# Kernel tuning notes

Measured on AMD Instinct MI355X. Metric: run time of the kernel, lower is better.

## Reference

```python
import jax, jax.numpy as jnp
import numpy as np

B, C, S, E, H = 16, 24, 128, 256, 8
P = E // H  # head projection dim (consistent interpretation of the buggy source)
EPS = 1e-6


def _ln(x, g, b):
    mu = jnp.mean(x, axis=-1, keepdims=True)
    var = jnp.mean((x - mu) ** 2, axis=-1, keepdims=True)
    return (x - mu) * jax.lax.rsqrt(var + EPS) * g + b


def setup_inputs() -> dict:
    key = jax.random.key(0)
    ks = jax.random.split(key, 16)
    s = 0.02
    return {
        'x': jax.random.normal(ks[0], (B, C, S, E), jnp.float32),
        # spatial attention params
        'Wq_s': s * jax.random.normal(ks[1], (H, C, P, E), jnp.float32),
        'Wk_s': s * jax.random.normal(ks[2], (H, E, P), jnp.float32),
        'Wv_s': s * jax.random.normal(ks[3], (H, E, P), jnp.float32),
        'Wo_s': s * jax.random.normal(ks[4], (C, E, E), jnp.float32),
        # temporal attention params
        'Wq_t': s * jax.random.normal(ks[5], (H, C, E, P), jnp.float32),
        'Wk_t': s * jax.random.normal(ks[6], (H, C, E, P), jnp.float32),
        'Wv_t': s * jax.random.normal(ks[7], (H, C, E, P), jnp.float32),
        'Wo_t': s * jax.random.normal(ks[8], (C, E, E), jnp.float32),
        # shared layernorm
        'ln_g': jnp.ones((E,), jnp.float32),
        'ln_b': jnp.zeros((E,), jnp.float32),
        # per-joint pointwise FF (Linear->ReLU->Linear)
        'ff_w1': s * jax.random.normal(ks[9], (C, E, E), jnp.float32),
        'ff_b1': jnp.zeros((C, E), jnp.float32),
        'ff_w2': s * jax.random.normal(ks[10], (C, E, E), jnp.float32),
        'ff_b2': jnp.zeros((C, E), jnp.float32),
    }


def _spatial_attention(x, Wq, Wk, Wv, Wo):
    # x: [B,C,S,E]; per-head per-joint query proj, shared key/value proj
    q = jnp.einsum('bcse,hcpe->bshcp', x, Wq)          # [B,S,H,C,P]
    k = jnp.einsum('bcse,hep->bshcp', x, Wk)
    v = jnp.einsum('bcse,hep->bshcp', x, Wv)
    scores = jnp.einsum('bshcp,bshdp->bshcd', q, k) / jnp.sqrt(jnp.float32(P))
    a = jax.nn.softmax(scores, axis=-1)                # attn over joints d
    o = jnp.einsum('bshcd,bshdp->bshcp', a, v)
    o = o.transpose(0, 3, 1, 2, 4).reshape(x.shape[0], C, x.shape[2], H * P)  # [B,C,S,E]
    return jnp.einsum('bcse,cef->bcsf', o, Wo)


def _temporal_attention(x, Wq, Wk, Wv, Wo):
    q = jnp.einsum('bcse,hcep->bhcsp', x, Wq)          # [B,H,C,S,P]
    k = jnp.einsum('bcse,hcep->bhcsp', x, Wk)
    v = jnp.einsum('bcse,hcep->bhcsp', x, Wv)
    scores = jnp.einsum('bhcsp,bhctp->bhcst', q, k) / jnp.sqrt(jnp.float32(P))
    a = jax.nn.softmax(scores, axis=-1)                # attn over time t
    o = jnp.einsum('bhcst,bhctp->bhcsp', a, v)
    o = o.transpose(0, 2, 3, 1, 4).reshape(x.shape[0], C, x.shape[2], H * P)  # [B,C,S,E]
    return jnp.einsum('bcse,cef->bcsf', o, Wo)


def reference(x, Wq_s, Wk_s, Wv_s, Wo_s, Wq_t, Wk_t, Wv_t, Wo_t, ln_g, ln_b, ff_w1, ff_b1, ff_w2, ff_b2):
    spat = _spatial_attention(x, Wq_s, Wk_s, Wv_s, Wo_s)
    temp = _temporal_attention(x, Wq_t, Wk_t, Wv_t, Wo_t)
    attn_out = _ln(x + spat, ln_g, ln_b) + _ln(x + temp, ln_g, ln_b)
    # per-joint pointwise FF, vectorized over joints
    h = jax.nn.relu(jnp.einsum('bcse,cef->bcsf', attn_out, ff_w1) + ff_b1[None, :, None, :])
    ff = jnp.einsum('bcse,cef->bcsf', h, ff_w2) + ff_b2[None, :, None, :]
    return _ln(attn_out + ff, ln_g, ln_b)
```

## Files before the change

### kernel.cpp

```cpp
#include <hip/hip_runtime.h>
#include <hip/hip_bf16.h>

constexpr int Bn = 16, Cn = 24, Sn = 128, En = 256, Hn = 8, Pn = 32;
constexpr int NROWS = Bn * Cn * Sn;
constexpr size_t NBUF = (size_t)Bn * Cn * Sn * En;
constexpr size_t WSLOT = (size_t)Cn * 256 * 256;

typedef __bf16 bf16_t;
typedef bf16_t bf16x8 __attribute__((ext_vector_type(8)));
typedef bf16_t bf16x4 __attribute__((ext_vector_type(4)));
typedef float f32x4 __attribute__((ext_vector_type(4)));

__device__ __forceinline__ void gl2lds16(const bf16_t* g, bf16_t* l) {
    typedef const __attribute__((address_space(1))) unsigned int* gp_t;
    typedef __attribute__((address_space(3))) unsigned int* lp_t;
    __builtin_amdgcn_global_load_lds((gp_t)(unsigned long long)g,
                                     (lp_t)(unsigned int)(unsigned long long)l,
                                     16, 0, 0);
}

__global__ __launch_bounds__(256) void conv_x_k(const float* __restrict__ x,
                                                bf16_t* __restrict__ xb) {
    const size_t i = ((size_t)blockIdx.x * 256 + threadIdx.x) * 4;
    const float4 v = *(const float4*)(x + i);
    bf16x4 o = {(bf16_t)v.x, (bf16_t)v.y, (bf16_t)v.z, (bf16_t)v.w};
    *(bf16x4*)(xb + i) = o;
}

__global__ __launch_bounds__(256) void conv_w_copy_k(const float* __restrict__ W,
                                                     bf16_t* __restrict__ out) {
    const int row = blockIdx.x * 4 + (threadIdx.x >> 6);
    const int lane = threadIdx.x & 63;
    const int n = row & 255, c = row >> 8;
    const float* src = W + (size_t)c * (Pn * En) + (size_t)(n >> 5) * (Cn * Pn * En) +
                       (size_t)(n & 31) * En + lane * 4;
    const float4 v = *(const float4*)src;
    bf16x4 o = {(bf16_t)v.x, (bf16_t)v.y, (bf16_t)v.z, (bf16_t)v.w};
    *(bf16x4*)(out + (size_t)row * 256 + lane * 4) = o;
}

struct TDesc { const float* W; int Sc, Snh, Se; };

__global__ __launch_bounds__(256) void conv_w_tr_k(
    TDesc d0, TDesc d1, TDesc d2, TDesc d3, TDesc d4, TDesc d5, TDesc d6,
    bf16_t* __restrict__ out)
{
    TDesc d;
    switch (blockIdx.z) {
        case 0: d = d0; break; case 1: d = d1; break; case 2: d = d2; break;
        case 3: d = d3; break; case 4: d = d4; break; case 5: d = d5; break;
        default: d = d6; break;
    }
    const int g = blockIdx.x & 7, et = blockIdx.x >> 3;
    const int c = blockIdx.y;

    __shared__ float tile[32][65];

    const int t = threadIdx.x;
    const float* base = d.W + (size_t)c * d.Sc + (size_t)g * d.Snh;

#pragma unroll
    for (int pass = 0; pass < 2; ++pass) {
        const int e_local = pass * 32 + (t >> 3);
        const int j4 = (t & 7) * 4;
        const float4 v = *(const float4*)(base + (size_t)(et * 64 + e_local) * d.Se + j4);
        tile[j4 + 0][e_local] = v.x;
        tile[j4 + 1][e_local] = v.y;
        tile[j4 + 2][e_local] = v.z;
        tile[j4 + 3][e_local] = v.w;
    }
    __syncthreads();

    const int j = t >> 3, e8 = (t & 7) * 8;
    bf16x8 o;
#pragma unroll
    for (int k = 0; k < 8; ++k) o[k] = (bf16_t)tile[j][e8 + k];
    *(bf16x8*)(out + (size_t)blockIdx.z * WSLOT +
               ((size_t)c * 256 + g * 32 + j) * 256 + et * 64 + e8) = o;
}

__global__ __launch_bounds__(256) void conv_w_k(const float* __restrict__ W,
                                                bf16_t* __restrict__ Wb,
                                                int Sc, int Snh, int Snp, int Se) {
    const int n = blockIdx.x & 255, c = blockIdx.x >> 8;
    const int e = threadIdx.x;
    Wb[(size_t)blockIdx.x * 256 + e] =
        (bf16_t)W[(size_t)c * Sc + (size_t)(n >> 5) * Snh + (n & 31) * Snp + (size_t)e * Se];
}

struct GDesc { const bf16_t* W; bf16_t* O; int Wc, Ob, Oc, Os, Onh, Onp, trans; };

template <int NP, int EPI>
__global__ __launch_bounds__(256) void gemm_mfma(
    const bf16_t* __restrict__ A, int Ab, int Ac, int As,
    GDesc g0, GDesc g1, GDesc g2, const float* __restrict__ bias)
{
    const int b = blockIdx.x, c = blockIdx.z;
    const int proj = (NP == 1) ? 0 : ((int)blockIdx.y >> 1);
    const int nt = (NP == 1) ? (int)blockIdx.y : ((int)blockIdx.y & 1);
    GDesc g = (proj == 0) ? g0 : (proj == 1) ? g1 : g2;

    __shared__ bf16_t smem[2][2][128 * 32];
    bf16_t* Cs = &smem[0][0][0];

    const int tid = threadIdx.x, wv = tid >> 6, ln = tid & 63;
    const int wm = (wv >> 1) * 64, wn = (wv & 1) * 64;
    const int lr = ln & 15, hi = ln >> 4, lk = hi * 8;

    const bf16_t* Abase = A + (size_t)b * Ab + (size_t)c * Ac;
    const bf16_t* Bbase = g.W + (size_t)c * g.Wc + (size_t)(nt * 128) * 256;

    auto stage = [&](int buf, int k0) {
#pragma unroll
        for (int it = 0; it < 2; ++it) {
            const int cb = it * 256 + wv * 64;
            const int mc = cb + ln;
            const int row = mc >> 2, kc = (mc & 3) * 8;
            gl2lds16(Abase + (size_t)row * As + k0 + kc, &smem[buf][0][cb * 8]);
            gl2lds16(Bbase + (size_t)row * 256 + k0 + kc, &smem[buf][1][cb * 8]);
        }
    };

    f32x4 acc[4][4] = {};

    stage(0, 0);
    __syncthreads();

#pragma unroll
    for (int kt = 0; kt < 8; ++kt) {
        const int cur = kt & 1;
        if (kt < 7) stage(cur ^ 1, (kt + 1) * 32);

        bf16x8 af[4], bfr[4];
#pragma unroll
        for (int i = 0; i < 4; ++i)
            af[i] = *(const bf16x8*)&smem[cur][0][(wm + i * 16 + lr) * 32 + lk];
#pragma unroll
        for (int j = 0; j < 4; ++j)
            bfr[j] = *(const bf16x8*)&smem[cur][1][(wn + j * 16 + lr) * 32 + lk];
#pragma unroll
        for (int i = 0; i < 4; ++i)
#pragma unroll
            for (int j = 0; j < 4; ++j)
                acc[i][j] = __builtin_amdgcn_mfma_f32_16x16x32_bf16(af[i], bfr[j], acc[i][j], 0, 0, 0);

        __syncthreads();
    }

#pragma unroll
    for (int pass = 0; pass < 2; ++pass) {
        if (!g.trans) {
            if (wm == pass * 64) {
#pragma unroll
                for (int i = 0; i < 4; ++i)
#pragma unroll
                    for (int j = 0; j < 4; ++j) {
                        const int n = nt * 128 + wn + j * 16 + lr;
                        float bv = 0.f;
                        if (EPI) bv = bias[c * 256 + n];
#pragma unroll
                        for (int r = 0; r < 4; ++r) {
                            float v = acc[i][j][r];
                            if (EPI) { v += bv; if (EPI == 1) v = fmaxf(v, 0.f); }
                            Cs[(i * 16 + hi * 4 + r) * 136 + wn + j * 16 + lr] = (bf16_t)v;
                        }
                    }
            }
            __syncthreads();
#pragma unroll
            for (int it = 0; it < 2; ++it) {
                const int lrow = it * 32 + (tid >> 3);
                const int n0 = (tid & 7) * 16;
                bf16x8 v0 = *(const bf16x8*)&Cs[lrow * 136 + n0];
                bf16x8 v1 = *(const bf16x8*)&Cs[lrow * 136 + n0 + 8];
                const int m = pass * 64 + lrow;
                const int n = nt * 128 + n0;
                bf16_t* dst = g.O + (size_t)b * g.Ob + (size_t)c * g.Oc +
                              (size_t)m * g.Os + (size_t)(n >> 5) * g.Onh + (n & 31);
                *(bf16x8*)dst = v0;
                *(bf16x8*)(dst + 8) = v1;
            }
            __syncthreads();
        } else {
            if (wn == pass * 64) {
#pragma unroll
                for (int i = 0; i < 4; ++i)
#pragma unroll
                    for (int j = 0; j < 4; ++j) {
                        bf16x4 pk = {(bf16_t)acc[i][j][0], (bf16_t)acc[i][j][1],
                                     (bf16_t)acc[i][j][2], (bf16_t)acc[i][j][3]};
                        *(bf16x4*)&Cs[(j * 16 + lr) * 136 + wm + i * 16 + hi * 4] = pk;
                    }
            }
            __syncthreads();
#pragma unroll
            for (int it = 0; it < 2; ++it) {
                const int lrow = it * 32 + (tid >> 3);
                const int m0 = (tid & 7) * 16;
                bf16x8 v0 = *(const bf16x8*)&Cs[lrow * 136 + m0];
                bf16x8 v1 = *(const bf16x8*)&Cs[lrow * 136 + m0 + 8];
                const int n = nt * 128 + pass * 64 + lrow;
                bf16_t* dst = g.O + (size_t)b * g.Ob + (size_t)c * g.Oc +
                              (size_t)(n >> 5) * g.Onh + (size_t)(n & 31) * g.Onp + m0;
                *(bf16x8*)dst = v0;
                *(bf16x8*)(dst + 8) = v1;
            }
            __syncthreads();
        }
    }
}

__global__ __launch_bounds__(256) void attn_spatial_mfma(
    const bf16_t* __restrict__ Q, const bf16_t* __restrict__ K,
    const bf16_t* __restrict__ V, bf16_t* __restrict__ O)
{
    __shared__ bf16_t Ps[4][32 * 40];
    __shared__ bf16_t Vt[4][32 * 40];

    const int tid = threadIdx.x, wv = tid >> 6, ln = tid & 63;
    const int lr = ln & 15, hi = ln >> 4, lk = hi * 8;

    const int bsh = blockIdx.x * 4 + wv;
    const int h = bsh & 7, s = (bsh >> 3) & 127, b = bsh >> 10;
    const size_t qb = (size_t)bsh * (Cn * Pn);

    {
        const int p = ln >> 1, c0 = 24 + (ln & 1) * 4;
        bf16x4 z = {};
        *(bf16x4*)&Vt[wv][p * 40 + c0] = z;
    }
#pragma unroll
    for (int it = 0; it < 2; ++it) {
        const int ch = it * 64 + ln;
        if (ch < 96) {
            const int cc = ch >> 2, p0 = (ch & 3) * 8;
            bf16x8 v = *(const bf16x8*)(V + qb + cc * 32 + p0);
#pragma unroll
            for (int j = 0; j < 8; ++j)
                Vt[wv][(p0 + j) * 40 + cc] = v[j];
        }
    }

    bf16x8 aq0 = *(const bf16x8*)(Q + qb + lr * 32 + lk);
    bf16x8 aq1 = *(const bf16x8*)(Q + qb + (16 + lr) * 32 + lk);
    bf16x8 bk0 = *(const bf16x8*)(K + qb + lr * 32 + lk);
    bf16x8 bk1 = *(const bf16x8*)(K + qb + (16 + lr) * 32 + lk);
    const f32x4 zz = {0.f, 0.f, 0.f, 0.f};
    f32x4 sc[2][2];
    sc[0][0] = __builtin_amdgcn_mfma_f32_16x16x32_bf16(aq0, bk0, zz, 0, 0, 0);
    sc[0][1] = __builtin_amdgcn_mfma_f32_16x16x32_bf16(aq0, bk1, zz, 0, 0, 0);
    sc[1][0] = __builtin_amdgcn_mfma_f32_16x16x32_bf16(aq1, bk0, zz, 0, 0, 0);
    sc[1][1] = __builtin_amdgcn_mfma_f32_16x16x32_bf16(aq1, bk1, zz, 0, 0, 0);

    const float scale = 0.17677669529663687f;
#pragma unroll
    for (int i = 0; i < 2; ++i) {
        float s0[4], s1[4], mx[4];
#pragma unroll
        for (int r = 0; r < 4; ++r) {
            s0[r] = sc[i][0][r] * scale;
            s1[r] = (lr >= 8) ? -3.0e38f : sc[i][1][r] * scale;
            mx[r] = fmaxf(s0[r], s1[r]);
        }
#pragma unroll
        for (int d = 1; d < 16; d <<= 1)
#pragma unroll
            for (int r = 0; r < 4; ++r) mx[r] = fmaxf(mx[r], __shfl_xor(mx[r], d));
        float e0[4], e1[4], sm[4];
#pragma unroll
        for (int r = 0; r < 4; ++r) {
            e0[r] = __expf(s0[r] - mx[r]);
            e1[r] = __expf(s1[r] - mx[r]);
            sm[r] = e0[r] + e1[r];
        }
#pragma unroll
        for (int d = 1; d < 16; d <<= 1)
#pragma unroll
            for (int r = 0; r < 4; ++r) sm[r] += __shfl_xor(sm[r], d);
#pragma unroll
        for (int r = 0; r < 4; ++r) {
            const float inv = 1.f / sm[r];
            const int row = i * 16 + hi * 4 + r;
            Ps[wv][row * 40 + lr]      = (bf16_t)(e0[r] * inv);
            Ps[wv][row * 40 + 16 + lr] = (bf16_t)(e1[r] * inv);
        }
    }

    bf16x8 ap0 = *(const bf16x8*)&Ps[wv][lr * 40 + lk];
    bf16x8 ap1 = *(const bf16x8*)&Ps[wv][(16 + lr) * 40 + lk];
    bf16x8 bv0 = *(const bf16x8*)&Vt[wv][lr * 40 + lk];
    bf16x8 bv1 = *(const bf16x8*)&Vt[wv][(16 + lr) * 40 + lk];
    f32x4 o[2][2];
    o[0][0] = __builtin_amdgcn_mfma_f32_16x16x32_bf16(ap0, bv0, zz, 0, 0, 0);
    o[0][1] = __builtin_amdgcn_mfma_f32_16x16x32_bf16(ap0, bv1, zz, 0, 0, 0);
    o[1][0] = __builtin_amdgcn_mfma_f32_16x16x32_bf16(ap1, bv0, zz, 0, 0, 0);
    o[1][1] = __builtin_amdgcn_mfma_f32_16x16x32_bf16(ap1, bv1, zz, 0, 0, 0);

#pragma unroll
    for (int i = 0; i < 2; ++i)
#pragma unroll
        for (int r = 0; r < 4; ++r) {
            const int c = i * 16 + hi * 4 + r;
            if (c < 24) {
                const size_t ob = ((size_t)(b * Cn + c) * Sn + s) * En + h * Pn;
#pragma unroll
                for (int j = 0; j < 2; ++j)
                    O[ob + j * 16 + lr] = (bf16_t)o[i][j][r];
            }
        }
}

__global__ __launch_bounds__(256) void attn_temporal_mfma(
    const bf16_t* __restrict__ Q, const bf16_t* __restrict__ K,
    const bf16_t* __restrict__ Vt, bf16_t* __restrict__ O)
{
    const int c = blockIdx.x, h = blockIdx.y, b = blockIdx.z;
    const size_t base = ((size_t)(b * Hn + h) * Cn + c) * (Sn * Pn);

    __shared__ bf16_t Qs[128 * 32];
    __shared__ bf16_t Ks[128 * 32];
    __shared__ bf16_t Vs[32 * 136];
    __shared__ bf16_t Ps[128 * 136];

    const int tid = threadIdx.x, wv = tid >> 6, ln = tid & 63;
    const int lr = ln & 15, lk = (ln >> 4) * 8;

#pragma unroll
    for (int it = 0; it < 2; ++it) {
        const int cb = it * 256 + wv * 64;
        const int mc = cb + ln;
        const int row = mc >> 2, kc = (mc & 3) * 8;
        gl2lds16(Q + base + row * 32 + kc, &Qs[cb * 8]);
        gl2lds16(K + base + row * 32 + kc, &Ks[cb * 8]);
    }
#pragma unroll
    for (int it = 0; it < 2; ++it) {
        const int mc = it * 256 + tid;
        const int p = mc >> 4, scn = (mc & 15) * 8;
        bf16x8 v = *(const bf16x8*)(Vt + base + p * 128 + scn);
        *(bf16x8*)&Vs[p * 136 + scn] = v;
    }
    __syncthreads();

    const int r0 = wv * 32;
    bf16x8 aq0 = *(const bf16x8*)&Qs[(r0 + lr) * 32 + lk];
    bf16x8 aq1 = *(const bf16x8*)&Qs[(r0 + 16 + lr) * 32 + lk];
    f32x4 sc_[2][8];
    const f32x4 zz = {0.f, 0.f, 0.f, 0.f};
#pragma unroll
    for (int j = 0; j < 8; ++j) {
        bf16x8 bk = *(const bf16x8*)&Ks[(j * 16 + lr) * 32 + lk];
        sc_[0][j] = __builtin_amdgcn_mfma_f32_16x16x32_bf16(aq0, bk, zz, 0, 0, 0);
        sc_[1][j] = __builtin_amdgcn_mfma_f32_16x16x32_bf16(aq1, bk, zz, 0, 0, 0);
    }

    const float scale = 0.17677669529663687f;
#pragma unroll
    for (int i = 0; i < 2; ++i) {
        float mx[4], sm[4];
#pragma unroll
        for (int r = 0; r < 4; ++r) {
            float m = sc_[i][0][r];
#pragma unroll
            for (int j = 1; j < 8; ++j) m = fmaxf(m, sc_[i][j][r]);
            mx[r] = m;
        }
#pragma unroll
        for (int d = 1; d < 16; d <<= 1)
#pragma unroll
            for (int r = 0; r < 4; ++r) mx[r] = fmaxf(mx[r], __shfl_xor(mx[r], d));
#pragma unroll
        for (int r = 0; r < 4; ++r) sm[r] = 0.f;
#pragma unroll
        for (int j = 0; j < 8; ++j)
#pragma unroll
            for (int r = 0; r < 4; ++r) {
                const float e = __expf((sc_[i][j][r] - mx[r]) * scale);
                sc_[i][j][r] = e; sm[r] += e;
            }
#pragma unroll
        for (int d = 1; d < 16; d <<= 1)
#pragma unroll
            for (int r = 0; r < 4; ++r) sm[r] += __shfl_xor(sm[r], d);
        float inv[4];
#pragma unroll
        for (int r = 0; r < 4; ++r) inv[r] = 1.f / sm[r];
        const int rb = r0 + i * 16 + (ln >> 4) * 4;
#pragma unroll
        for (int j = 0; j < 8; ++j)
#pragma unroll
            for (int r = 0; r < 4; ++r)
                Ps[(rb + r) * 136 + j * 16 + lr] = (bf16_t)(sc_[i][j][r] * inv[r]);
    }
    __syncthreads();

    f32x4 o[2][2] = {};
#pragma unroll
    for (int kk = 0; kk < 4; ++kk) {
        bf16x8 ap0 = *(const bf16x8*)&Ps[(r0 + lr) * 136 + kk * 32 + lk];
        bf16x8 ap1 = *(const bf16x8*)&Ps[(r0 + 16 + lr) * 136 + kk * 32 + lk];
        bf16x8 bv0 = *(const bf16x8*)&Vs[lr * 136 + kk * 32 + lk];
        bf16x8 bv1 = *(const bf16x8*)&Vs[(16 + lr) * 136 + kk * 32 + lk];
        o[0][0] = __builtin_amdgcn_mfma_f32_16x16x32_bf16(ap0, bv0, o[0][0], 0, 0, 0);
        o[0][1] = __builtin_amdgcn_mfma_f32_16x16x32_bf16(ap0, bv1, o[0][1], 0, 0, 0);
        o[1][0] = __builtin_amdgcn_mfma_f32_16x16x32_bf16(ap1, bv0, o[1][0], 0, 0, 0);
        o[1][1] = __builtin_amdgcn_mfma_f32_16x16x32_bf16(ap1, bv1, o[1][1], 0, 0, 0);
    }

#pragma unroll
    for (int i = 0; i < 2; ++i) {
        const int sb = r0 + i * 16 + (ln >> 4) * 4;
#pragma unroll
        for (int j = 0; j < 2; ++j) {
            const int p = h * 32 + j * 16 + lr;
#pragma unroll
            for (int r = 0; r < 4; ++r)
                O[((size_t)(b * Cn + c) * Sn + (sb + r)) * En + p] = (bf16_t)o[i][j][r];
        }
    }
}

__global__ __launch_bounds__(256) void ln_combine_k(
    const bf16_t* __restrict__ xb, const bf16_t* __restrict__ spat,
    const bf16_t* __restrict__ temp, const float* __restrict__ g,
    const float* __restrict__ beta, bf16_t* __restrict__ AO)
{
    const int row = blockIdx.x * 4 + (threadIdx.x >> 6);
    const int lane = threadIdx.x & 63;
    const size_t off = (size_t)row * En;

    float v1[4], v2[4];
    float s1 = 0, s2 = 0, q1 = 0, q2 = 0;
#pragma unroll
    for (int i = 0; i < 4; i++) {
        const int e = lane + i * 64;
        const float xv = (float)xb[off + e];
        const float a = xv + (float)spat[off + e];
        const float t = xv + (float)temp[off + e];
        v1[i] = a; v2[i] = t;
        s1 += a; s2 += t; q1 += a * a; q2 += t * t;
    }
    for (int d = 32; d; d >>= 1) {
        s1 += __shfl_xor(s1, d); s2 += __shfl_xor(s2, d);
        q1 += __shfl_xor(q1, d); q2 += __shfl_xor(q2, d);
    }
    const float mu1 = s1 / En, mu2 = s2 / En;
    const float r1 = rsqrtf(q1 / En - mu1 * mu1 + 1e-6f);
    const float r2 = rsqrtf(q2 / En - mu2 * mu2 + 1e-6f);
#pragma unroll
    for (int i = 0; i < 4; i++) {
        const int e = lane + i * 64;
        const float out = (v1[i] - mu1) * r1 * g[e] + beta[e] +
                          (v2[i] - mu2) * r2 * g[e] + beta[e];
        AO[off + e] = (bf16_t)out;
    }
}

__global__ __launch_bounds__(256) void ln_final_k(
    const bf16_t* __restrict__ AO, const bf16_t* __restrict__ FF,
    const float* __restrict__ g, const float* __restrict__ beta,
    float* __restrict__ out)
{
    const int row = blockIdx.x * 4 + (threadIdx.x >> 6);
    const int lane = threadIdx.x & 63;
    const size_t off = (size_t)row * En;

    float v[4];
    float s = 0, q = 0;
#pragma unroll
    for (int i = 0; i < 4; i++) {
        const int e = lane + i * 64;
        const float a = (float)AO[off + e] + (float)FF[off + e];
        v[i] = a; s += a; q += a * a;
    }
    for (int d = 32; d; d >>= 1) { s += __shfl_xor(s, d); q += __shfl_xor(q, d); }
    const float mu = s / En;
    const float r = rsqrtf(q / En - mu * mu + 1e-6f);
#pragma unroll
    for (int i = 0; i < 4; i++) {
        const int e = lane + i * 64;
        out[off + e] = (v[i] - mu) * r * g[e] + beta[e];
    }
}

extern "C" void kernel_launch(void* const* d_in, const int* in_sizes, int n_in,
                              void* d_out, int out_size, void* d_ws, size_t ws_size,
                              hipStream_t stream)
{
    const float* x     = (const float*)d_in[0];
    const float* Wq_s  = (const float*)d_in[1];
    const float* Wk_s  = (const float*)d_in[2];
    const float* Wv_s  = (const float*)d_in[3];
    const float* Wo_s  = (const float*)d_in[4];
    const float* Wq_t  = (const float*)d_in[5];
    const float* Wk_t  = (const float*)d_in[6];
    const float* Wv_t  = (const float*)d_in[7];
    const float* Wo_t  = (const float*)d_in[8];
    const float* ln_g  = (const float*)d_in[9];
    const float* ln_b  = (const float*)d_in[10];
    const float* ff_w1 = (const float*)d_in[11];
    const float* ff_b1 = (const float*)d_in[12];
    const float* ff_w2 = (const float*)d_in[13];
    const float* ff_b2 = (const float*)d_in[14];
    float* out = (float*)d_out;

    bf16_t* wsb = (bf16_t*)d_ws;
    bf16_t* b0 = wsb;
    bf16_t* b1 = wsb + NBUF;
    bf16_t* b2 = wsb + 2 * NBUF;
    bf16_t* b3 = wsb + 3 * NBUF;
    bf16_t* b4 = wsb + 4 * NBUF;

    bf16_t* xb = (bf16_t*)d_out;
    bf16_t* wb = xb + NBUF;
    bf16_t* w_qs = wb + 0 * WSLOT;
    bf16_t* wtr  = wb + 1 * WSLOT;
    bf16_t* w_os = wtr + 0 * WSLOT;
    bf16_t* w_qt = wtr + 1 * WSLOT;
    bf16_t* w_kt = wtr + 2 * WSLOT;
    bf16_t* w_vt = wtr + 3 * WSLOT;
    bf16_t* w_ot = wtr + 4 * WSLOT;
    bf16_t* w_f1 = wtr + 5 * WSLOT;
    bf16_t* w_f2 = wtr + 6 * WSLOT;
    bf16_t* w_ks = b4 + NBUF - 2 * 65536;
    bf16_t* w_vs = b4 + NBUF - 65536;

    const int XAb = Cn * Sn * En, XAc = Sn * En, XAs = En;
    const int QSb = Sn * Hn * Cn * Pn, QSs = Hn * Cn * Pn, QSh = Cn * Pn;
    const int QTb = Hn * Cn * Sn * Pn, QTh = Cn * Sn * Pn, QTc = Sn * Pn, QTs = Pn;
    const int WCP = 256 * 256;

    conv_x_k<<<NBUF / 1024, 256, 0, stream>>>(x, xb);
    conv_w_copy_k<<<1536, 256, 0, stream>>>(Wq_s, w_qs);
    conv_w_tr_k<<<dim3(32, 24, 7), 256, 0, stream>>>(
        TDesc{Wo_s, En * En, Pn, En},
        TDesc{Wq_t, En * Pn, Cn * En * Pn, Pn},
        TDesc{Wk_t, En * Pn, Cn * En * Pn, Pn},
        TDesc{Wv_t, En * Pn, Cn * En * Pn, Pn},
        TDesc{Wo_t, En * En, Pn, En},
        TDesc{ff_w1, En * En, Pn, En},
        TDesc{ff_w2, En * En, Pn, En},
        wtr);
    conv_w_k<<<256, 256, 0, stream>>>(Wk_s, w_ks, 0, En * Pn, 1, Pn);
    conv_w_k<<<256, 256, 0, stream>>>(Wv_s, w_vs, 0, En * Pn, 1, Pn);

    gemm_mfma<3, 0><<<dim3(16, 6, 24), 256, 0, stream>>>(
        xb, XAb, XAc, XAs,
        GDesc{w_qs, b0, WCP, QSb, Pn, QSs, QSh, 1, 0},
        GDesc{w_ks, b1, 0,   QSb, Pn, QSs, QSh, 1, 0},
        GDesc{w_vs, b2, 0,   QSb, Pn, QSs, QSh, 1, 0},
        nullptr);
    attn_spatial_mfma<<<Bn * Sn * Hn / 4, 256, 0, stream>>>(b0, b1, b2, b3);
    gemm_mfma<1, 0><<<dim3(16, 2, 24), 256, 0, stream>>>(
        b3, XAb, XAc, XAs,
        GDesc{w_os, b4, WCP, XAb, XAc, XAs, 32, 1, 0},
        GDesc{w_os, b4, WCP, XAb, XAc, XAs, 32, 1, 0},
        GDesc{w_os, b4, WCP, XAb, XAc, XAs, 32, 1, 0}, nullptr);

    gemm_mfma<3, 0><<<dim3(16, 6, 24), 256, 0, stream>>>(
        xb, XAb, XAc, XAs,
        GDesc{w_qt, b0, WCP, QTb, QTc, QTs, QTh, 1, 0},
        GDesc{w_kt, b1, WCP, QTb, QTc, QTs, QTh, 1, 0},
        GDesc{w_vt, b2, WCP, QTb, QTc, 1, QTh, Sn, 1},
        nullptr);
    attn_temporal_mfma<<<dim3(24, 8, 16), 256, 0, stream>>>(b0, b1, b2, b3);
    gemm_mfma<1, 0><<<dim3(16, 2, 24), 256, 0, stream>>>(
        b3, XAb, XAc, XAs,
        GDesc{w_ot, b0, WCP, XAb, XAc, XAs, 32, 1, 0},
        GDesc{w_ot, b0, WCP, XAb, XAc, XAs, 32, 1, 0},
        GDesc{w_ot, b0, WCP, XAb, XAc, XAs, 32, 1, 0}, nullptr);

    ln_combine_k<<<NROWS / 4, 256, 0, stream>>>(xb, b4, b0, ln_g, ln_b, b1);
    gemm_mfma<1, 1><<<dim3(16, 2, 24), 256, 0, stream>>>(
        b1, XAb, XAc, XAs,
        GDesc{w_f1, b2, WCP, XAb, XAc, XAs, 32, 1, 0},
        GDesc{w_f1, b2, WCP, XAb, XAc, XAs, 32, 1, 0},
        GDesc{w_f1, b2, WCP, XAb, XAc, XAs, 32, 1, 0}, ff_b1);
    gemm_mfma<1, 2><<<dim3(16, 2, 24), 256, 0, stream>>>(
        b2, XAb, XAc, XAs,
        GDesc{w_f2, b3, WCP, XAb, XAc, XAs, 32, 1, 0},
        GDesc{w_f2, b3, WCP, XAb, XAc, XAs, 32, 1, 0},
        GDesc{w_f2, b3, WCP, XAb, XAc, XAs, 32, 1, 0}, ff_b2);
    ln_final_k<<<NROWS / 4, 256, 0, stream>>>(b1, b3, ln_g, ln_b, out);
}
```

Measured before the change: 413.3 us.

## Triple-buffer GEMM K-loop and merge the two attention output projections

The bf16 MFMA GEMM moves from a double-buffered to a triple-buffered LDS pipeline that prefetches two K-tiles ahead. It uses explicit vmcnt waits and raw s_barriers in place of __syncthreads, and raises wave priority around the MFMA block. The spatial and temporal output-projection GEMMs now run as one NP=2 launch, selected by a new per-descriptor A offset, which saves a launch and improves grid fill. The cost is more LDS per block (48KB), which may lower occupancy. The merged launch also assumes the temporal attention output buffer sits exactly NBUF elements after the spatial one.

```diff
diff --git a/kernel.cpp b/kernel.cpp
--- a/kernel.cpp
+++ b/kernel.cpp
@@ -88,7 +88,7 @@
         (bf16_t)W[(size_t)c * Sc + (size_t)(n >> 5) * Snh + (n & 31) * Snp + (size_t)e * Se];
 }
 
-struct GDesc { const bf16_t* W; bf16_t* O; int Wc, Ob, Oc, Os, Onh, Onp, trans; };
+struct GDesc { const bf16_t* W; bf16_t* O; int Aoff, Wc, Ob, Oc, Os, Onh, Onp, trans; };
 
 template <int NP, int EPI>
 __global__ __launch_bounds__(256) void gemm_mfma(
@@ -100,17 +100,18 @@
     const int nt = (NP == 1) ? (int)blockIdx.y : ((int)blockIdx.y & 1);
     GDesc g = (proj == 0) ? g0 : (proj == 1) ? g1 : g2;
 
-    __shared__ bf16_t smem[2][2][128 * 32];
+    __shared__ bf16_t smem[3][2][128 * 32];
     bf16_t* Cs = &smem[0][0][0];
 
     const int tid = threadIdx.x, wv = tid >> 6, ln = tid & 63;
     const int wm = (wv >> 1) * 64, wn = (wv & 1) * 64;
     const int lr = ln & 15, hi = ln >> 4, lk = hi * 8;
 
-    const bf16_t* Abase = A + (size_t)b * Ab + (size_t)c * Ac;
+    const bf16_t* Abase = A + g.Aoff + (size_t)b * Ab + (size_t)c * Ac;
     const bf16_t* Bbase = g.W + (size_t)c * g.Wc + (size_t)(nt * 128) * 256;
 
-    auto stage = [&](int buf, int k0) {
+    auto stage = [&](int buf, int kt) {
+        const int k0 = kt * 32;
 #pragma unroll
         for (int it = 0; it < 2; ++it) {
             const int cb = it * 256 + wv * 64;
@@ -124,13 +125,18 @@
     f32x4 acc[4][4] = {};
 
     stage(0, 0);
-    __syncthreads();
+    stage(1, 1);
 
 #pragma unroll
     for (int kt = 0; kt < 8; ++kt) {
-        const int cur = kt & 1;
-        if (kt < 7) stage(cur ^ 1, (kt + 1) * 32);
-
+        if (kt < 6) stage((kt + 2) % 3, kt + 2);
+        if (kt < 6)       asm volatile("s_waitcnt vmcnt(8)" ::: "memory");
+        else if (kt == 6) asm volatile("s_waitcnt vmcnt(4)" ::: "memory");
+        else              asm volatile("s_waitcnt vmcnt(0)" ::: "memory");
+        __builtin_amdgcn_s_barrier();
+        __builtin_amdgcn_sched_barrier(0);
+
+        const int cur = kt % 3;
         bf16x8 af[4], bfr[4];
 #pragma unroll
         for (int i = 0; i < 4; ++i)
@@ -138,13 +144,16 @@
 #pragma unroll
         for (int j = 0; j < 4; ++j)
             bfr[j] = *(const bf16x8*)&smem[cur][1][(wn + j * 16 + lr) * 32 + lk];
+        __builtin_amdgcn_s_setprio(1);
 #pragma unroll
         for (int i = 0; i < 4; ++i)
 #pragma unroll
             for (int j = 0; j < 4; ++j)
                 acc[i][j] = __builtin_amdgcn_mfma_f32_16x16x32_bf16(af[i], bfr[j], acc[i][j], 0, 0, 0);
-
-        __syncthreads();
+        __builtin_amdgcn_s_setprio(0);
+
+        __builtin_amdgcn_sched_barrier(0);
+        __builtin_amdgcn_s_barrier();
     }
 
 #pragma unroll
@@ -546,40 +555,36 @@
 
     gemm_mfma<3, 0><<<dim3(16, 6, 24), 256, 0, stream>>>(
         xb, XAb, XAc, XAs,
-        GDesc{w_qs, b0, WCP, QSb, Pn, QSs, QSh, 1, 0},
-        GDesc{w_ks, b1, 0,   QSb, Pn, QSs, QSh, 1, 0},
-        GDesc{w_vs, b2, 0,   QSb, Pn, QSs, QSh, 1, 0},
+        GDesc{w_qs, b0, 0, WCP, QSb, Pn, QSs, QSh, 1, 0},
+        GDesc{w_ks, b1, 0, 0,   QSb, Pn, QSs, QSh, 1, 0},
+        GDesc{w_vs, b2, 0, 0,   QSb, Pn, QSs, QSh, 1, 0},
         nullptr);
     attn_spatial_mfma<<<Bn * Sn * Hn / 4, 256, 0, stream>>>(b0, b1, b2, b3);
-    gemm_mfma<1, 0><<<dim3(16, 2, 24), 256, 0, stream>>>(
-        b3, XAb, XAc, XAs,
-        GDesc{w_os, b4, WCP, XAb, XAc, XAs, 32, 1, 0},
-        GDesc{w_os, b4, WCP, XAb, XAc, XAs, 32, 1, 0},
-        GDesc{w_os, b4, WCP, XAb, XAc, XAs, 32, 1, 0}, nullptr);
 
     gemm_mfma<3, 0><<<dim3(16, 6, 24), 256, 0, stream>>>(
         xb, XAb, XAc, XAs,
-        GDesc{w_qt, b0, WCP, QTb, QTc, QTs, QTh, 1, 0},
-        GDesc{w_kt, b1, WCP, QTb, QTc, QTs, QTh, 1, 0},
-        GDesc{w_vt, b2, WCP, QTb, QTc, 1, QTh, Sn, 1},
+        GDesc{w_qt, b0, 0, WCP, QTb, QTc, QTs, QTh, 1, 0},
+        GDesc{w_kt, b1, 0, WCP, QTb, QTc, QTs, QTh, 1, 0},
+        GDesc{w_vt, b2, 0, WCP, QTb, QTc, 1, QTh, Sn, 1},
         nullptr);
-    attn_temporal_mfma<<<dim3(24, 8, 16), 256, 0, stream>>>(b0, b1, b2, b3);
-    gemm_mfma<1, 0><<<dim3(16, 2, 24), 256, 0, stream>>>(
+    attn_temporal_mfma<<<dim3(24, 8, 16), 256, 0, stream>>>(b0, b1, b2, b4);
+
+    gemm_mfma<2, 0><<<dim3(16, 4, 24), 256, 0, stream>>>(
         b3, XAb, XAc, XAs,
-        GDesc{w_ot, b0, WCP, XAb, XAc, XAs, 32, 1, 0},
-        GDesc{w_ot, b0, WCP, XAb, XAc, XAs, 32, 1, 0},
-        GDesc{w_ot, b0, WCP, XAb, XAc, XAs, 32, 1, 0}, nullptr);
-
-    ln_combine_k<<<NROWS / 4, 256, 0, stream>>>(xb, b4, b0, ln_g, ln_b, b1);
+        GDesc{w_os, b0, 0,          WCP, XAb, XAc, XAs, 32, 1, 0},
+        GDesc{w_ot, b1, (int)NBUF,  WCP, XAb, XAc, XAs, 32, 1, 0},
+        GDesc{w_os, b0, 0,          WCP, XAb, XAc, XAs, 32, 1, 0}, nullptr);
+
+    ln_combine_k<<<NROWS / 4, 256, 0, stream>>>(xb, b0, b1, ln_g, ln_b, b2);
     gemm_mfma<1, 1><<<dim3(16, 2, 24), 256, 0, stream>>>(
-        b1, XAb, XAc, XAs,
-        GDesc{w_f1, b2, WCP, XAb, XAc, XAs, 32, 1, 0},
-        GDesc{w_f1, b2, WCP, XAb, XAc, XAs, 32, 1, 0},
-        GDesc{w_f1, b2, WCP, XAb, XAc, XAs, 32, 1, 0}, ff_b1);
+        b2, XAb, XAc, XAs,
+        GDesc{w_f1, b3, 0, WCP, XAb, XAc, XAs, 32, 1, 0},
+        GDesc{w_f1, b3, 0, WCP, XAb, XAc, XAs, 32, 1, 0},
+        GDesc{w_f1, b3, 0, WCP, XAb, XAc, XAs, 32, 1, 0}, ff_b1);
     gemm_mfma<1, 2><<<dim3(16, 2, 24), 256, 0, stream>>>(
-        b2, XAb, XAc, XAs,
-        GDesc{w_f2, b3, WCP, XAb, XAc, XAs, 32, 1, 0},
-        GDesc{w_f2, b3, WCP, XAb, XAc, XAs, 32, 1, 0},
-        GDesc{w_f2, b3, WCP, XAb, XAc, XAs, 32, 1, 0}, ff_b2);
-    ln_final_k<<<NROWS / 4, 256, 0, stream>>>(b1, b3, ln_g, ln_b, out);
-}
+        b3, XAb, XAc, XAs,
+        GDesc{w_f2, b4, 0, WCP, XAb, XAc, XAs, 32, 1, 0},
+        GDesc{w_f2, b4, 0, WCP, XAb, XAc, XAs, 32, 1, 0},
+        GDesc{w_f2, b4, 0, WCP, XAb, XAc, XAs, 32, 1, 0}, ff_b2);
+    ln_final_k<<<NROWS / 4, 256, 0, stream>>>(b2, b4, ln_g, ln_b, out);
+}
```

After: 387.8 us. -6.2%, faster.
